# Kernel optimization log

Measured on AMD Instinct MI355X. Metric: run time of the kernel, lower is better.

The kernel has to match this reference:

```python
import jax, jax.numpy as jnp
import numpy as np

DIM = 512
HEADS = 8
LANDMARKS = 64


def setup_inputs() -> dict:
    key = jax.random.key(0)
    ks = jax.random.split(key, 9)
    B, N, C = 2, 16384, DIM
    s = 0.02
    return {
        "x": jax.random.normal(ks[0], (B, N, C), dtype=jnp.float32),
        "wq": jax.random.normal(ks[1], (C, C), dtype=jnp.float32) * s,
        "bq": jnp.zeros((C,), dtype=jnp.float32),
        "wk": jax.random.normal(ks[2], (C, C), dtype=jnp.float32) * s,
        "bk": jnp.zeros((C,), dtype=jnp.float32),
        "wv": jax.random.normal(ks[3], (C, C), dtype=jnp.float32) * s,
        "bv": jnp.zeros((C,), dtype=jnp.float32),
        "wo": jax.random.normal(ks[4], (C, C), dtype=jnp.float32) * s,
        "bo": jnp.zeros((C,), dtype=jnp.float32),
    }


def _to_heads(x, H):
    B, N, C = x.shape
    return x.reshape(B, N, H, C // H).transpose(0, 2, 1, 3)  # (B,H,N,hd)


def reference(x, wq, bq, wk, bk, wv, bv, wo, bo):
    B, N, C = x.shape
    H = HEADS
    hd = C // H
    scale = hd ** (-0.5)
    m = min(LANDMARKS, N)

    q = _to_heads(x @ wq.T + bq, H) * scale  # (B,H,N,hd)
    k = _to_heads(x @ wk.T + bk, H)
    v = _to_heads(x @ wv.T + bv, H)

    if N <= m * 2:
        attn = jax.nn.softmax(jnp.einsum("bhnd,bhkd->bhnk", q, k), axis=-1)
        out = jnp.einsum("bhnk,bhkd->bhnd", attn, v)
    else:
        seg = (N + m - 1) // m
        pad = seg * m - N
        if pad > 0:
            q_p = jnp.pad(q, ((0, 0), (0, 0), (0, pad), (0, 0)))
            k_p = jnp.pad(k, ((0, 0), (0, 0), (0, pad), (0, 0)))
        else:
            q_p, k_p = q, k
        # landmarks: mean over consecutive segments of length seg (zero-pad included, as in torch)
        q_land = q_p.reshape(B, H, m, seg, hd).mean(3)  # (B,H,m,hd)
        k_land = k_p.reshape(B, H, m, seg, hd).mean(3)

        ker1 = jax.nn.softmax(jnp.einsum("bhnd,bhmd->bhnm", q, k_land), axis=-1)  # (B,H,N,m)
        ker2 = jax.nn.softmax(jnp.einsum("bhld,bhmd->bhlm", q_land, k_land), axis=-1)  # (B,H,m,m)
        ker3 = jax.nn.softmax(jnp.einsum("bhmd,bhnd->bhmn", q_land, k), axis=-1)  # (B,H,m,N)
        ker2_inv = jnp.linalg.pinv(ker2)  # (B,H,m,m)

        kv = jnp.einsum("bhmn,bhnd->bhmd", ker3, v)  # (B,H,m,hd)
        out = jnp.einsum("bhnm,bhmd->bhnd", ker1, ker2_inv @ kv)

    out = out.transpose(0, 2, 1, 3).reshape(B, N, C)
    return out @ wo.T + bo
```

## Files before the change

kernel.cpp:

```cpp
#include <hip/hip_runtime.h>
#include <stdint.h>


constexpr int B_   = 2;
constexpr int N_   = 16384;
constexpr int C_   = 512;
constexpr int H_   = 8;
constexpr int HD_  = 64;
constexpr int LM_  = 64;
constexpr int SEG_ = 256;
constexpr int BH_  = 16;
constexpr int NCH_ = 16;
constexpr int NPART_ = 64;
constexpr int SW1_ = 3;
constexpr int SW2_ = 2;

#define RCOND_ (640.0 * 1.1920928955078125e-07)

typedef unsigned short ushort4_t __attribute__((ext_vector_type(4)));
typedef unsigned short ushort8_t __attribute__((ext_vector_type(8)));
typedef __bf16 bf16x8 __attribute__((ext_vector_type(8)));
typedef float f32x4 __attribute__((ext_vector_type(4)));

__device__ inline float bf2f(unsigned short u) {
  union { unsigned int i; float f; } x; x.i = ((unsigned int)u) << 16; return x.f;
}
__device__ inline unsigned short f2bf(float f) {
  union { float f; unsigned int i; } x; x.f = f;
  unsigned int lsb = (x.i >> 16) & 1;
  return (unsigned short)((x.i + 0x7fffu + lsb) >> 16);
}
__device__ inline bf16x8 ld_bf8(const unsigned short* p) { return *(const bf16x8*)p; }

__device__ __forceinline__ void gload_lds16(const unsigned short* gsrc, unsigned short* ldst) {
  __builtin_amdgcn_global_load_lds((const __attribute__((address_space(1))) void*)gsrc,
                                   (__attribute__((address_space(3))) void*)ldst, 16, 0, 0);
}

__global__ __launch_bounds__(256) void cvt_w4_kernel(const float* __restrict__ wq,
                                                     const float* __restrict__ wk,
                                                     const float* __restrict__ wv,
                                                     const float* __restrict__ wo,
                                                     unsigned short* __restrict__ dq,
                                                     unsigned short* __restrict__ dk,
                                                     unsigned short* __restrict__ dv,
                                                     unsigned short* __restrict__ dwo) {
  int which = blockIdx.y;
  const float* src = which == 0 ? wq : which == 1 ? wk : which == 2 ? wv : wo;
  unsigned short* dst = which == 0 ? dq : which == 1 ? dk : which == 2 ? dv : dwo;
  int i = blockIdx.x * 256 + threadIdx.x;
  const float* s = src + (size_t)i * 8;
  float4 x0 = *(const float4*)(s);
  float4 x1 = *(const float4*)(s + 4);
  ushort8_t u;
  u[0] = f2bf(x0.x); u[1] = f2bf(x0.y); u[2] = f2bf(x0.z); u[3] = f2bf(x0.w);
  u[4] = f2bf(x1.x); u[5] = f2bf(x1.y); u[6] = f2bf(x1.z); u[7] = f2bf(x1.w);
  *(ushort8_t*)(dst + (size_t)i * 8) = u;
}

__global__ __launch_bounds__(512) void seg_mean_kernel(const float* __restrict__ x,
                                                       float* __restrict__ xbar,
                                                       unsigned short* __restrict__ xb) {
  int bl = blockIdx.x;
  int b = bl / LM_, l = bl % LM_;
  int t = threadIdx.x;
  int c4 = t & 127;
  int rq = t >> 7;
  const size_t rowbase = (size_t)b * N_ + (size_t)l * SEG_;
  const float* xp = x + rowbase * C_;
  float4 s = make_float4(0.f, 0.f, 0.f, 0.f);
  for (int r = rq * 64; r < rq * 64 + 64; ++r) {
    float4 v = *(const float4*)(xp + (size_t)r * C_ + c4 * 4);
    s.x += v.x; s.y += v.y; s.z += v.z; s.w += v.w;
    ushort4_t u;
    u[0] = f2bf(v.x); u[1] = f2bf(v.y); u[2] = f2bf(v.z); u[3] = f2bf(v.w);
    *(ushort4_t*)(xb + (rowbase + r) * C_ + c4 * 4) = u;
  }
  __shared__ float red[4][512];
  *(float4*)&red[rq][c4 * 4] = s;
  __syncthreads();
  if (rq == 0) {
    float4 a0 = *(float4*)&red[0][c4 * 4];
    float4 a1 = *(float4*)&red[1][c4 * 4];
    float4 a2 = *(float4*)&red[2][c4 * 4];
    float4 a3 = *(float4*)&red[3][c4 * 4];
    const float invs = 1.0f / SEG_;
    float4 o;
    o.x = ((a0.x + a1.x) + (a2.x + a3.x)) * invs;
    o.y = ((a0.y + a1.y) + (a2.y + a3.y)) * invs;
    o.z = ((a0.z + a1.z) + (a2.z + a3.z)) * invs;
    o.w = ((a0.w + a1.w) + (a2.w + a3.w)) * invs;
    *(float4*)(xbar + (size_t)bl * C_ + c4 * 4) = o;
  }
}

__global__ __launch_bounds__(256) void land_gemm_kernel(const float* __restrict__ xbar,
                                                        const float* __restrict__ wq,
                                                        const float* __restrict__ bq,
                                                        const float* __restrict__ wk,
                                                        const float* __restrict__ bk,
                                                        float* __restrict__ qland,
                                                        float* __restrict__ kland,
                                                        unsigned short* __restrict__ qlbh,
                                                        unsigned short* __restrict__ qlbl,
                                                        unsigned short* __restrict__ klb) {
  __shared__ float As[32][68];
  __shared__ float Ws[32][68];
  int which = blockIdx.x >> 1;
  int row0 = (blockIdx.x & 1) * 64;
  int col0 = blockIdx.y * 64;
  const float* A = xbar;
  const float* W = which ? wk : wq;
  const float* bias = which ? bk : bq;
  float scale = which ? 1.0f : 0.125f;
  float* out = which ? kland : qland;
  int tid = threadIdx.x;
  int tm = tid >> 4, tn = tid & 15;
  float acc[4][4] = {};
  for (int k0 = 0; k0 < C_; k0 += 32) {
#pragma unroll
    for (int i = 0; i < 2; ++i) {
      int s = tid + i * 256;
      int r = s >> 3;
      int kg = (s & 7) << 2;
      float4 av = *(const float4*)(A + (size_t)(row0 + r) * C_ + k0 + kg);
      As[kg + 0][r] = av.x; As[kg + 1][r] = av.y;
      As[kg + 2][r] = av.z; As[kg + 3][r] = av.w;
      float4 wv = *(const float4*)(W + (size_t)(col0 + r) * C_ + k0 + kg);
      Ws[kg + 0][r] = wv.x; Ws[kg + 1][r] = wv.y;
      Ws[kg + 2][r] = wv.z; Ws[kg + 3][r] = wv.w;
    }
    __syncthreads();
#pragma unroll
    for (int kk = 0; kk < 32; ++kk) {
      float4 a = *(const float4*)&As[kk][tm * 4];
      float4 b = *(const float4*)&Ws[kk][tn * 4];
      float av[4] = {a.x, a.y, a.z, a.w};
      float bv[4] = {b.x, b.y, b.z, b.w};
#pragma unroll
      for (int i = 0; i < 4; ++i)
#pragma unroll
        for (int j = 0; j < 4; ++j) acc[i][j] += av[i] * bv[j];
    }
    __syncthreads();
  }
#pragma unroll
  for (int i = 0; i < 4; ++i) {
    int row = row0 + tm * 4 + i;
    int d0 = tn * 4;
    float o4[4];
#pragma unroll
    for (int j = 0; j < 4; ++j) o4[j] = (acc[i][j] + bias[col0 + d0 + j]) * scale;
    int b = row / LM_, n = row % LM_;
    int h = col0 >> 6;
    size_t idx = (((size_t)(b * H_ + h) * LM_) + n) * HD_ + d0;
    float4 o; o.x = o4[0]; o.y = o4[1]; o.z = o4[2]; o.w = o4[3];
    *(float4*)(out + idx) = o;
    if (which == 0) {
      ushort4_t uh, ul;
#pragma unroll
      for (int j = 0; j < 4; ++j) {
        unsigned short hbits = f2bf(o4[j]);
        uh[j] = hbits;
        ul[j] = f2bf(o4[j] - bf2f(hbits));
      }
      *(ushort4_t*)(qlbh + idx) = uh;
      *(ushort4_t*)(qlbl + idx) = ul;
    } else {
      ushort4_t uk;
#pragma unroll
      for (int j = 0; j < 4; ++j) uk[j] = f2bf(o4[j]);
      *(ushort4_t*)(klb + idx) = uk;
    }
  }
}

__device__ __forceinline__ void dma_gemm_body(const unsigned short* __restrict__ A,
                                              const unsigned short* __restrict__ W,
                                              const float* __restrict__ bias,
                                              void* __restrict__ out,
                                              float scale, int omode,
                                              int row0, int col0,
                                              unsigned short* Xs, unsigned short* Wl,
                                              int tid) {
  int w = tid >> 6, lane = tid & 63;
  int wr = w >> 1, wc = w & 1;
  f32x4 acc[4][4] = {};

  for (int k0 = 0; k0 < C_; k0 += 64) {
    __syncthreads();
#pragma unroll
    for (int i = 0; i < 4; ++i) {
      int r = i * 32 + w * 8 + (lane >> 3);
      int c8 = (lane & 7) * 8;
      gload_lds16(A + (size_t)(row0 + r) * C_ + k0 + c8, &Xs[(i * 32 + w * 8) * 64]);
      gload_lds16(W + (size_t)(col0 + r) * C_ + k0 + c8, &Wl[(i * 32 + w * 8) * 64]);
    }
    __syncthreads();
    bf16x8 af[4][2], bfr[4][2];
#pragma unroll
    for (int m = 0; m < 4; ++m) {
      af[m][0] = *(bf16x8*)&Xs[(wr * 64 + m * 16 + (lane & 15)) * 64 + (lane >> 4) * 8];
      af[m][1] = *(bf16x8*)&Xs[(wr * 64 + m * 16 + (lane & 15)) * 64 + 32 + (lane >> 4) * 8];
    }
#pragma unroll
    for (int n = 0; n < 4; ++n) {
      bfr[n][0] = *(bf16x8*)&Wl[(wc * 64 + n * 16 + (lane & 15)) * 64 + (lane >> 4) * 8];
      bfr[n][1] = *(bf16x8*)&Wl[(wc * 64 + n * 16 + (lane & 15)) * 64 + 32 + (lane >> 4) * 8];
    }
#pragma unroll
    for (int ks = 0; ks < 2; ++ks)
#pragma unroll
      for (int m = 0; m < 4; ++m)
#pragma unroll
        for (int n = 0; n < 4; ++n)
          acc[m][n] = __builtin_amdgcn_mfma_f32_16x16x32_bf16(af[m][ks], bfr[n][ks], acc[m][n], 0, 0, 0);
  }

#pragma unroll
  for (int m = 0; m < 4; ++m) {
    int rbase = row0 + wr * 64 + m * 16 + (lane >> 4) * 4;
#pragma unroll
    for (int n = 0; n < 4; ++n) {
      int c = col0 + wc * 64 + n * 16 + (lane & 15);
      float bc = bias[c];
      if (omode == 0) {
#pragma unroll
        for (int rg = 0; rg < 4; ++rg)
          ((float*)out)[(size_t)(rbase + rg) * C_ + c] = acc[m][n][rg] + bc;
      } else if (omode == 2) {
        int b = rbase >> 14, nn = rbase & 16383;
        int h = c >> 6, d = c & 63;
        ushort4_t u;
#pragma unroll
        for (int rg = 0; rg < 4; ++rg) u[rg] = f2bf((acc[m][n][rg] + bc) * scale);
        *(ushort4_t*)((unsigned short*)out + ((size_t)(b * H_ + h) * HD_ + d) * N_ + nn) = u;
      } else {
#pragma unroll
        for (int rg = 0; rg < 4; ++rg) {
          float val = (acc[m][n][rg] + bc) * scale;
          int r = rbase + rg;
          int b = r >> 14, nn = r & 16383, h = c >> 6, d = c & 63;
          ((unsigned short*)out)[(((size_t)(b * H_ + h) * N_) + nn) * HD_ + d] = f2bf(val);
        }
      }
    }
  }
}

template <int NW>
__device__ __forceinline__ void svd_sweeps(float* a, float* v, char* smemraw,
                                           int w, int lane, int nsweeps) {
  constexpr int RP = 64 / NW;
  float (*Ac)[68] = (float(*)[68])(smemraw);
  float (*Vc)[68] = (float(*)[68])(smemraw + 17408);
  float (*pg)[NW][64] = (float(*)[NW][64])(smemraw + 34816);
  float (*pa)[64] = (float(*)[64])(smemraw + 34816 + 2 * NW * 64 * 4);
  const int r0 = w * RP;
#pragma unroll
  for (int c = 0; c < RP; c += 4) {
    *(float4*)&Ac[lane][r0 + c] = make_float4(a[c], a[c + 1], a[c + 2], a[c + 3]);
    *(float4*)&Vc[lane][r0 + c] = make_float4(v[c], v[c + 1], v[c + 2], v[c + 3]);
  }

  for (int sweep = 0; sweep < nsweeps; ++sweep) {
    float p0 = 0.f, p1 = 0.f;
#pragma unroll
    for (int k = 0; k < RP; k += 2) { p0 = fmaf(a[k], a[k], p0); p1 = fmaf(a[k + 1], a[k + 1], p1); }
    pa[w][lane] = p0 + p1;
    __syncthreads();
    float alpha;
    if constexpr (NW == 4)
      alpha = (pa[0][lane] + pa[1][lane]) + (pa[2][lane] + pa[3][lane]);
    else
      alpha = ((pa[0][lane] + pa[1][lane]) + (pa[2][lane] + pa[3][lane])) +
              ((pa[4][lane] + pa[5][lane]) + (pa[6][lane] + pa[7][lane]));
    for (int mask = 1; mask < 64; ++mask) {
      int buf = mask & 1;
      int partner = lane ^ mask;
      bool lower = lane < partner;
      float beta = __shfl_xor(alpha, mask);
      float o[RP];
#pragma unroll
      for (int c = 0; c < RP; c += 4) {
        float4 t4 = *(float4*)&Ac[partner][r0 + c];
        o[c] = t4.x; o[c + 1] = t4.y; o[c + 2] = t4.z; o[c + 3] = t4.w;
      }
      float g0 = 0.f, g1 = 0.f;
#pragma unroll
      for (int k = 0; k < RP; k += 2) { g0 = fmaf(a[k], o[k], g0); g1 = fmaf(a[k + 1], o[k + 1], g1); }
      pg[buf][w][lane] = g0 + g1;
      __syncthreads();
      float gamma;
      if constexpr (NW == 4)
        gamma = (pg[buf][0][lane] + pg[buf][1][lane]) + (pg[buf][2][lane] + pg[buf][3][lane]);
      else
        gamma = ((pg[buf][0][lane] + pg[buf][1][lane]) + (pg[buf][2][lane] + pg[buf][3][lane])) +
                ((pg[buf][4][lane] + pg[buf][5][lane]) + (pg[buf][6][lane] + pg[buf][7][lane]));
      bool need = (gamma * gamma > 1e-12f * alpha * beta);
      if (__any(need)) {
        float ov[RP];
#pragma unroll
        for (int c = 0; c < RP; c += 4) {
          float4 t4 = *(float4*)&Vc[partner][r0 + c];
          ov[c] = t4.x; ov[c + 1] = t4.y; ov[c + 2] = t4.z; ov[c + 3] = t4.w;
        }
        float ap = lower ? alpha : beta;
        float aq = lower ? beta : alpha;
        float c = 1.f, s = 0.f;
        if (need) {
          float tau = (aq - ap) / (2.f * gamma);
          float t = copysignf(1.f, tau) / (fabsf(tau) + sqrtf(fmaf(tau, tau, 1.f)));
          c = rsqrtf(fmaf(t, t, 1.f));
          s = t * c;
        }
        float sm = lower ? -s : s;
#pragma unroll
        for (int k = 0; k < RP; ++k) a[k] = fmaf(sm, o[k], c * a[k]);
#pragma unroll
        for (int k = 0; k < RP; ++k) v[k] = fmaf(sm, ov[k], c * v[k]);
        float twocsg = 2.f * c * s * gamma;
        alpha = fmaf(c * c, alpha, fmaf(s * s, beta, lower ? -twocsg : twocsg));
#pragma unroll
        for (int cc = 0; cc < RP; cc += 4) {
          *(float4*)&Ac[lane][r0 + cc] = make_float4(a[cc], a[cc + 1], a[cc + 2], a[cc + 3]);
          *(float4*)&Vc[lane][r0 + cc] = make_float4(v[cc], v[cc + 1], v[cc + 2], v[cc + 3]);
        }
      }
    }
  }
}

__device__ void svd_phase1(const float* __restrict__ qland, const float* __restrict__ kland,
                           float* __restrict__ asave, float* __restrict__ vsave,
                           int bh, char* smemraw, int tid) {
  __builtin_amdgcn_s_setprio(3);
  float (*qlS)[65] = (float(*)[65])(smemraw);
  float (*klS)[65] = (float(*)[65])(smemraw + 16640);
  for (int i = 0; i < 2; ++i) {
    int s = tid + i * 512;
    int r = s >> 4, d4 = (s & 15) << 2;
    *(float4*)&qlS[r][d4] = *(const float4*)(qland + ((size_t)bh * 64 + r) * 64 + d4);
    *(float4*)&klS[r][d4] = *(const float4*)(kland + ((size_t)bh * 64 + r) * 64 + d4);
  }
  __syncthreads();
  int w = tid >> 6, lane = tid & 63;
  float a[8], v[8];
#pragma unroll
  for (int k = 0; k < 8; ++k) {
    int row = w * 8 + k;
    float acc = 0.f;
#pragma unroll
    for (int d4 = 0; d4 < 64; d4 += 4) {
      float4 qv = *(float4*)&qlS[row][d4];
      float4 kv = *(float4*)&klS[lane][d4];
      acc += qv.x * kv.x + qv.y * kv.y + qv.z * kv.z + qv.w * kv.w;
    }
    float e = expf(acc);
    float rs = e;
#pragma unroll
    for (int m = 1; m < 64; m <<= 1) rs += __shfl_xor(rs, m);
    a[k] = e * (1.f / rs);
  }
#pragma unroll
  for (int k = 0; k < 8; ++k) v[k] = (w * 8 + k == lane) ? 1.f : 0.f;
  __syncthreads();
  svd_sweeps<8>(a, v, smemraw, w, lane, SW1_);
#pragma unroll
  for (int k = 0; k < 8; ++k) {
    asave[((size_t)bh * 64 + w * 8 + k) * 64 + lane] = a[k];
    vsave[((size_t)bh * 64 + w * 8 + k) * 64 + lane] = v[k];
  }
  __builtin_amdgcn_s_setprio(0);
}

__device__ void svd_phase2(const float* __restrict__ asave, const float* __restrict__ vsave,
                           float* __restrict__ pinv, int bh, char* smemraw, int tid) {
  __builtin_amdgcn_s_setprio(3);
  double (*ps2)[64]  = (double(*)[64])(smemraw + 40960);
  float (*vsL)[65]   = (float(*)[65])(smemraw);
  float (*wasL)[65]  = (float(*)[65])(smemraw + 16640);
  int w = tid >> 6, lane = tid & 63;
  float a[8], v[8];
#pragma unroll
  for (int k = 0; k < 8; ++k) {
    a[k] = asave[((size_t)bh * 64 + w * 8 + k) * 64 + lane];
    v[k] = vsave[((size_t)bh * 64 + w * 8 + k) * 64 + lane];
  }
  svd_sweeps<8>(a, v, smemraw, w, lane, SW2_);

  double psig = 0.0;
#pragma unroll
  for (int k = 0; k < 8; ++k) psig += (double)a[k] * (double)a[k];
  ps2[w][lane] = psig;
  __syncthreads();
  double sig2 = ((ps2[0][lane] + ps2[1][lane]) + (ps2[2][lane] + ps2[3][lane])) +
                ((ps2[4][lane] + ps2[5][lane]) + (ps2[6][lane] + ps2[7][lane]));
  double smax = sig2;
#pragma unroll
  for (int m = 1; m < 64; m <<= 1) smax = fmax(smax, __shfl_xor(smax, m));
  double cutoff2 = smax * (RCOND_ * RCOND_);
  float wgt = (sig2 > cutoff2) ? (float)(1.0 / sig2) : 0.f;

#pragma unroll
  for (int k = 0; k < 8; ++k) {
    vsL[lane][w * 8 + k] = v[k];
    wasL[lane][w * 8 + k] = wgt * a[k];
  }
  __syncthreads();
  int i = tid >> 3;
  int j0 = (tid & 7) * 8;
  float acc[8] = {};
  for (int r = 0; r < 64; ++r) {
    float vv = vsL[r][i];
#pragma unroll
    for (int jj = 0; jj < 8; ++jj) acc[jj] = fmaf(vv, wasL[r][j0 + jj], acc[jj]);
  }
#pragma unroll
  for (int jj = 0; jj < 8; jj += 4) {
    float4 ovv = make_float4(acc[jj], acc[jj + 1], acc[jj + 2], acc[jj + 3]);
    *(float4*)(pinv + ((size_t)bh * 64 + i) * 64 + j0 + jj) = ovv;
  }
  __builtin_amdgcn_s_setprio(0);
}

__global__ __launch_bounds__(512) void fused1_kernel(
    const unsigned short* __restrict__ xb,
    const unsigned short* __restrict__ wqb, const float* __restrict__ bq,
    const unsigned short* __restrict__ wkb, const float* __restrict__ bk,
    const unsigned short* __restrict__ wvb, const float* __restrict__ bv,
    unsigned short* __restrict__ q4, unsigned short* __restrict__ k4,
    unsigned short* __restrict__ vt,
    const float* __restrict__ qland, const float* __restrict__ kland,
    float* __restrict__ asave, float* __restrict__ vsave) {
  __shared__ __align__(16) char smem[65536];
  int tid = threadIdx.x;
  int blk = blockIdx.x;
  if (blk < 16) { svd_phase1(qland, kland, asave, vsave, blk, smem, tid); return; }
  int g = blk - 16;
  int which = g >> 9;
  int subpair = g & 511;
  int half = tid >> 8;
  int ltid = tid & 255;
  int sub = subpair * 2 + half;
  int row0 = (sub >> 2) * 128;
  int col0 = (sub & 3) * 128;
  unsigned short* Xs = (unsigned short*)(smem + half * 32768);
  unsigned short* Wl = Xs + 128 * 64;
  if (which == 0)
    dma_gemm_body(xb, wqb, bq, q4, 0.125f, 1, row0, col0, Xs, Wl, ltid);
  else if (which == 1)
    dma_gemm_body(xb, wkb, bk, k4, 1.0f, 1, row0, col0, Xs, Wl, ltid);
  else
    dma_gemm_body(xb, wvb, bv, vt, 1.0f, 2, row0, col0, Xs, Wl, ltid);
}

__device__ void ker3kv_body(const unsigned short* __restrict__ qlh,
                            const unsigned short* __restrict__ qll,
                            const unsigned short* __restrict__ k4,
                            const unsigned short* __restrict__ vt,
                            float* __restrict__ pacc,
                            float* __restrict__ pacc0,
                            float* __restrict__ ps,
                            int bh, int ch, char* smemraw, int tid) {
  int w = tid >> 6, lane = tid & 63;
  int part = ch * 4 + w;
  int lrow = lane & 15, lgrp = lane >> 4;
  unsigned short* myP = (unsigned short*)smemraw + w * 64 * 72;

  bf16x8 qah[4][2], qal[4][2];
#pragma unroll
  for (int mf = 0; mf < 4; ++mf)
#pragma unroll
    for (int ks = 0; ks < 2; ++ks) {
      size_t off = ((size_t)bh * 64 + mf * 16 + lrow) * 64 + ks * 32 + lgrp * 8;
      qah[mf][ks] = ld_bf8(qlh + off);
      qal[mf][ks] = ld_bf8(qll + off);
    }
  bf16x8 onesf;
#pragma unroll
  for (int j = 0; j < 8; ++j) onesf[j] = (__bf16)1.0f;

  f32x4 kvacc[4][4] = {};
  f32x4 oneacc[4] = {};
  f32x4 ssum[4] = {};

  for (int sub = 0; sub < 4; ++sub) {
    int n0 = ch * 1024 + w * 256 + sub * 64;
    f32x4 sacc[4][4] = {};
#pragma unroll
    for (int ks = 0; ks < 2; ++ks) {
#pragma unroll
      for (int nf = 0; nf < 4; ++nf) {
        bf16x8 kb = ld_bf8(k4 + ((size_t)bh * N_ + n0 + nf * 16 + lrow) * 64 + ks * 32 + lgrp * 8);
#pragma unroll
        for (int mf = 0; mf < 4; ++mf) {
          sacc[mf][nf] = __builtin_amdgcn_mfma_f32_16x16x32_bf16(qah[mf][ks], kb, sacc[mf][nf], 0, 0, 0);
          sacc[mf][nf] = __builtin_amdgcn_mfma_f32_16x16x32_bf16(qal[mf][ks], kb, sacc[mf][nf], 0, 0, 0);
        }
      }
    }
#pragma unroll
    for (int mf = 0; mf < 4; ++mf) {
#pragma unroll
      for (int nf = 0; nf < 4; ++nf) {
#pragma unroll
        for (int r = 0; r < 4; ++r) {
          float pd = expf(sacc[mf][nf][r]) - 1.0f;
          ssum[mf][r] += pd;
          myP[(mf * 16 + lgrp * 4 + r) * 72 + nf * 16 + lrow] = f2bf(pd);
        }
      }
    }
#pragma unroll
    for (int ks = 0; ks < 2; ++ks) {
      bf16x8 pa[4];
#pragma unroll
      for (int mf = 0; mf < 4; ++mf)
        pa[mf] = ld_bf8(myP + (mf * 16 + lrow) * 72 + ks * 32 + lgrp * 8);
#pragma unroll
      for (int nf = 0; nf < 4; ++nf) {
        bf16x8 vb = ld_bf8(vt + ((size_t)bh * 64 + nf * 16 + lrow) * N_ + n0 + ks * 32 + lgrp * 8);
#pragma unroll
        for (int mf = 0; mf < 4; ++mf)
          kvacc[mf][nf] = __builtin_amdgcn_mfma_f32_16x16x32_bf16(pa[mf], vb, kvacc[mf][nf], 0, 0, 0);
        oneacc[nf] = __builtin_amdgcn_mfma_f32_16x16x32_bf16(onesf, vb, oneacc[nf], 0, 0, 0);
      }
    }
  }
#pragma unroll
  for (int mf = 0; mf < 4; ++mf)
#pragma unroll
    for (int m = 1; m < 16; m <<= 1)
#pragma unroll
      for (int r = 0; r < 4; ++r) ssum[mf][r] += __shfl_xor(ssum[mf][r], m);

  size_t pb = (((size_t)bh * NPART_ + part) * 64) * 64;
#pragma unroll
  for (int mf = 0; mf < 4; ++mf)
#pragma unroll
    for (int nf = 0; nf < 4; ++nf)
#pragma unroll
      for (int r = 0; r < 4; ++r)
        pacc[pb + (size_t)(mf * 16 + lgrp * 4 + r) * 64 + nf * 16 + lrow] = kvacc[mf][nf][r];
  if (lrow == 0) {
#pragma unroll
    for (int mf = 0; mf < 4; ++mf)
#pragma unroll
      for (int r = 0; r < 4; ++r)
        ps[((size_t)bh * NPART_ + part) * 64 + mf * 16 + lgrp * 4 + r] = ssum[mf][r];
  }
  if (lgrp == 0) {
#pragma unroll
    for (int nf = 0; nf < 4; ++nf)
      pacc0[((size_t)bh * NPART_ + part) * 64 + nf * 16 + lrow] = oneacc[nf][0];
  }
}

__global__ __launch_bounds__(512, 1) void fused2_kernel(
    const unsigned short* __restrict__ qlh,
    const unsigned short* __restrict__ qll,
    const unsigned short* __restrict__ k4,
    const unsigned short* __restrict__ vt,
    float* __restrict__ pacc, float* __restrict__ pacc0, float* __restrict__ ps,
    const float* __restrict__ asave, const float* __restrict__ vsave,
    float* __restrict__ pinv) {
  __shared__ __align__(16) char smem[73728];
  int tid = threadIdx.x;
  int blk = blockIdx.x;
  if (blk < 16) { svd_phase2(asave, vsave, pinv, blk, smem, tid); return; }
  int g = blk - 16;
  int bh = g >> 3, cpair = g & 7;
  int half = tid >> 8;
  int ltid = tid & 255;
  int ch = cpair * 2 + half;
  ker3kv_body(qlh, qll, k4, vt, pacc, pacc0, ps, bh, ch, smem + half * 36864, ltid);
}

__global__ __launch_bounds__(256) void cm_kernel(const float* __restrict__ pacc,
                                                 const float* __restrict__ pacc0,
                                                 const float* __restrict__ ps,
                                                 const float* __restrict__ pinv,
                                                 unsigned short* __restrict__ mtbh,
                                                 unsigned short* __restrict__ mtbl,
                                                 float* __restrict__ msum) {
  int bh = blockIdx.x;
  int tid = threadIdx.x;
  __shared__ float kvs[64][68];
  __shared__ double pcsd[64];
  for (int g = 0; g < 4; ++g) {
    int lm = g * 16 + (tid >> 4);
    int d4 = (tid & 15) * 4;
    float s = 16384.f;
    for (int part = 0; part < NPART_; ++part) s += ps[((size_t)bh * NPART_ + part) * 64 + lm];
    float4 a = make_float4(0.f, 0.f, 0.f, 0.f);
    for (int part = 0; part < NPART_; ++part) {
      float4 c0 = *(const float4*)&pacc0[((size_t)bh * NPART_ + part) * 64 + d4];
      float4 v = *(const float4*)&pacc[(((size_t)bh * NPART_ + part) * 64 + lm) * 64 + d4];
      a.x += c0.x + v.x; a.y += c0.y + v.y; a.z += c0.z + v.z; a.w += c0.w + v.w;
    }
    float inv = 1.f / s;
    kvs[lm][d4 + 0] = a.x * inv; kvs[lm][d4 + 1] = a.y * inv;
    kvs[lm][d4 + 2] = a.z * inv; kvs[lm][d4 + 3] = a.w * inv;
  }
  if (tid < 64) {
    double s = 0.0;
    for (int l = 0; l < 64; ++l) s += (double)pinv[((size_t)bh * 64 + l) * 64 + tid];
    pcsd[tid] = s;
  }
  __syncthreads();
  int l = tid >> 2, t = tid & 3;
  double o[16] = {};
  for (int j = 0; j < 64; ++j) {
    double pv = (double)pinv[((size_t)bh * 64 + l) * 64 + j];
#pragma unroll
    for (int i = 0; i < 16; ++i) o[i] += pv * (double)kvs[j][t * 16 + i];
  }
#pragma unroll
  for (int i = 0; i < 16; ++i) {
    float f = (float)o[i];
    unsigned short hi = f2bf(f);
    float lo = f - bf2f(hi);
    int d = t * 16 + i;
    mtbh[((size_t)bh * 64 + d) * 64 + l] = hi;
    mtbl[((size_t)bh * 64 + d) * 64 + l] = f2bf(lo);
  }
  if (tid < 64) {
    double m = 0.0;
    for (int j = 0; j < 64; ++j) m += pcsd[j] * (double)kvs[j][tid];
    msum[(size_t)bh * 64 + tid] = (float)(m * (1.0 / 64.0));
  }
}

__global__ __launch_bounds__(256, 1) void ker1out_mfma_kernel(
    const unsigned short* __restrict__ q4,
    const unsigned short* __restrict__ klb,
    const unsigned short* __restrict__ mtbh,
    const unsigned short* __restrict__ mtbl,
    const float* __restrict__ msum,
    unsigned short* __restrict__ outh) {
  int bh = blockIdx.y, tile = blockIdx.x;
  int b = bh >> 3, h = bh & 7;
  int tid = threadIdx.x, w = tid >> 6, lane = tid & 63;
  int lrow = lane & 15, lgrp = lane >> 4;
  int tok0 = tile * 256 + w * 64;
  __shared__ __align__(16) unsigned short Pl[4][64 * 72];
  unsigned short* myP = &Pl[w][0];

  f32x4 sacc[4][4] = {};
#pragma unroll
  for (int ks = 0; ks < 2; ++ks) {
    bf16x8 kb[4];
#pragma unroll
    for (int nf = 0; nf < 4; ++nf)
      kb[nf] = ld_bf8(klb + ((size_t)bh * 64 + nf * 16 + lrow) * 64 + ks * 32 + lgrp * 8);
#pragma unroll
    for (int mf = 0; mf < 4; ++mf) {
      bf16x8 qa = ld_bf8(q4 + ((size_t)bh * N_ + tok0 + mf * 16 + lrow) * 64 + ks * 32 + lgrp * 8);
#pragma unroll
      for (int nf = 0; nf < 4; ++nf)
        sacc[mf][nf] = __builtin_amdgcn_mfma_f32_16x16x32_bf16(qa, kb[nf], sacc[mf][nf], 0, 0, 0);
    }
  }
  f32x4 ssum[4] = {};
#pragma unroll
  for (int mf = 0; mf < 4; ++mf)
#pragma unroll
    for (int nf = 0; nf < 4; ++nf)
#pragma unroll
      for (int r = 0; r < 4; ++r) {
        sacc[mf][nf][r] = expf(sacc[mf][nf][r]);
        ssum[mf][r] += sacc[mf][nf][r];
      }
#pragma unroll
  for (int mf = 0; mf < 4; ++mf)
#pragma unroll
    for (int m = 1; m < 16; m <<= 1)
#pragma unroll
      for (int r = 0; r < 4; ++r) ssum[mf][r] += __shfl_xor(ssum[mf][r], m);
#pragma unroll
  for (int mf = 0; mf < 4; ++mf) {
    f32x4 inv;
#pragma unroll
    for (int r = 0; r < 4; ++r) inv[r] = 1.f / ssum[mf][r];
#pragma unroll
    for (int nf = 0; nf < 4; ++nf)
#pragma unroll
      for (int r = 0; r < 4; ++r) {
        float pdev = fmaf(sacc[mf][nf][r], inv[r], -0.015625f);
        myP[(mf * 16 + lgrp * 4 + r) * 72 + nf * 16 + lrow] = f2bf(pdev);
      }
  }

  f32x4 oacc[4][4] = {};
#pragma unroll
  for (int ks = 0; ks < 2; ++ks) {
    bf16x8 pa[4];
#pragma unroll
    for (int mf = 0; mf < 4; ++mf)
      pa[mf] = ld_bf8(myP + (mf * 16 + lrow) * 72 + ks * 32 + lgrp * 8);
#pragma unroll
    for (int nf = 0; nf < 4; ++nf) {
      bf16x8 mh = ld_bf8(mtbh + ((size_t)bh * 64 + nf * 16 + lrow) * 64 + ks * 32 + lgrp * 8);
      bf16x8 ml = ld_bf8(mtbl + ((size_t)bh * 64 + nf * 16 + lrow) * 64 + ks * 32 + lgrp * 8);
#pragma unroll
      for (int mf = 0; mf < 4; ++mf) {
        oacc[mf][nf] = __builtin_amdgcn_mfma_f32_16x16x32_bf16(pa[mf], mh, oacc[mf][nf], 0, 0, 0);
        oacc[mf][nf] = __builtin_amdgcn_mfma_f32_16x16x32_bf16(pa[mf], ml, oacc[mf][nf], 0, 0, 0);
      }
    }
  }
#pragma unroll
  for (int nf = 0; nf < 4; ++nf) {
    float ms = msum[(size_t)bh * 64 + nf * 16 + lrow];
#pragma unroll
    for (int mf = 0; mf < 4; ++mf)
#pragma unroll
      for (int r = 0; r < 4; ++r) {
        int tok = tok0 + mf * 16 + lgrp * 4 + r;
        int d = nf * 16 + lrow;
        outh[((size_t)b * N_ + tok) * C_ + h * HD_ + d] = f2bf(oacc[mf][nf][r] + ms);
      }
  }
}

__global__ __launch_bounds__(256) void oproj_kernel(const unsigned short* __restrict__ outh,
                                                    const unsigned short* __restrict__ wob,
                                                    const float* __restrict__ bo,
                                                    float* __restrict__ out) {
  __shared__ __align__(16) unsigned short Xs[128 * 64];
  __shared__ __align__(16) unsigned short Wl[128 * 64];
  dma_gemm_body(outh, wob, bo, out, 1.0f, 0, blockIdx.x * 128, blockIdx.y * 128,
                Xs, Wl, threadIdx.x);
}

extern "C" void kernel_launch(void* const* d_in, const int* in_sizes, int n_in,
                              void* d_out, int out_size, void* d_ws, size_t ws_size,
                              hipStream_t stream) {
  const float* x  = (const float*)d_in[0];
  const float* wq = (const float*)d_in[1];
  const float* bq = (const float*)d_in[2];
  const float* wk = (const float*)d_in[3];
  const float* bk = (const float*)d_in[4];
  const float* wv = (const float*)d_in[5];
  const float* bv = (const float*)d_in[6];
  const float* wo = (const float*)d_in[7];
  const float* bo = (const float*)d_in[8];
  float* out = (float*)d_out;

  char* base = (char*)d_ws;
  const size_t QKV = (size_t)BH_ * N_ * HD_;
  unsigned short* q4 = (unsigned short*)base;
  unsigned short* k4 = (unsigned short*)(base + QKV * 2);
  unsigned short* vt = (unsigned short*)(base + QKV * 4);
  unsigned short* outh = (unsigned short*)(base + QKV * 2);
  char* sp = base + QKV * 6;
  float* pacc  = (float*)sp; sp += (size_t)BH_ * NPART_ * 64 * 64 * 4;
  float* pacc0 = (float*)sp; sp += (size_t)BH_ * NPART_ * 64 * 4;
  float* ps    = (float*)sp; sp += (size_t)BH_ * NPART_ * 64 * 4;
  float* xbar  = (float*)sp; sp += (size_t)B_ * LM_ * C_ * 4;
  float* qland = (float*)sp; sp += (size_t)BH_ * LM_ * HD_ * 4;
  float* kland = (float*)sp; sp += (size_t)BH_ * LM_ * HD_ * 4;
  unsigned short* qlbh = (unsigned short*)sp; sp += (size_t)BH_ * LM_ * HD_ * 2;
  unsigned short* qlbl = (unsigned short*)sp; sp += (size_t)BH_ * LM_ * HD_ * 2;
  unsigned short* klb  = (unsigned short*)sp; sp += (size_t)BH_ * LM_ * HD_ * 2;
  float* pinv  = (float*)sp; sp += (size_t)BH_ * LM_ * LM_ * 4;
  unsigned short* mtbh = (unsigned short*)sp; sp += (size_t)BH_ * LM_ * HD_ * 2;
  unsigned short* mtbl = (unsigned short*)sp; sp += (size_t)BH_ * LM_ * HD_ * 2;
  float* msum  = (float*)sp; sp += (size_t)BH_ * HD_ * 4;
  float* asave = (float*)sp; sp += (size_t)BH_ * LM_ * LM_ * 4;
  float* vsave = (float*)sp; sp += (size_t)BH_ * LM_ * LM_ * 4;
  unsigned short* wob = (unsigned short*)sp; sp += (size_t)C_ * C_ * 2;
  unsigned short* wqb = (unsigned short*)sp; sp += (size_t)C_ * C_ * 2;
  unsigned short* wkb = (unsigned short*)sp; sp += (size_t)C_ * C_ * 2;
  unsigned short* wvb = (unsigned short*)sp; sp += (size_t)C_ * C_ * 2;

  unsigned short* xb = (unsigned short*)d_out;

  const int W8 = (C_ * C_) / 8;

  dim3 gc(W8 / 256, 4);
  cvt_w4_kernel<<<gc, 256, 0, stream>>>(wq, wk, wv, wo, wqb, wkb, wvb, wob);

  seg_mean_kernel<<<B_ * LM_, 512, 0, stream>>>(x, xbar, xb);
  dim3 gl(4, 8);
  land_gemm_kernel<<<gl, 256, 0, stream>>>(xbar, wq, bq, wk, bk,
                                           qland, kland, qlbh, qlbl, klb);

  fused1_kernel<<<16 + 3 * 512, 512, 0, stream>>>(
      xb, wqb, bq, wkb, bk, wvb, bv, q4, k4, vt, qland, kland, asave, vsave);

  fused2_kernel<<<16 + BH_ * 8, 512, 0, stream>>>(
      qlbh, qlbl, k4, vt, pacc, pacc0, ps, asave, vsave, pinv);

  cm_kernel<<<BH_, 256, 0, stream>>>(pacc, pacc0, ps, pinv, mtbh, mtbl, msum);

  dim3 g9(N_ / 256, BH_);
  ker1out_mfma_kernel<<<g9, 256, 0, stream>>>(q4, klb, mtbh, mtbl, msum, outh);

  dim3 g10(B_ * N_ / 128, C_ / 128);
  oproj_kernel<<<g10, 256, 0, stream>>>(outh, wob, bo, out);
}
```

Measured before the change: 385.6 us.

## Split seg-mean across columns, swizzle GEMM LDS, shuffle-based Jacobi SVD

Three separate changes. The segment-mean kernel now launches four times as many 128-thread blocks, each covering a quarter of the columns, to get more parallelism across CUs. The DMA GEMM applies an XOR swizzle to the column position in the LDS tiles so fragment reads avoid bank conflicts. The Jacobi SVD sweeps now exchange partner columns with wavefront shuffles instead of round-tripping through shared-memory arrays, which removes the LDS stores and loads inside each rotation but adds more shuffle instructions.

```diff
diff --git a/kernel.cpp b/kernel.cpp
--- a/kernel.cpp
+++ b/kernel.cpp
@@ -58,25 +58,27 @@
   *(ushort8_t*)(dst + (size_t)i * 8) = u;
 }
 
-__global__ __launch_bounds__(512) void seg_mean_kernel(const float* __restrict__ x,
+__global__ __launch_bounds__(128) void seg_mean_kernel(const float* __restrict__ x,
                                                        float* __restrict__ xbar,
                                                        unsigned short* __restrict__ xb) {
-  int bl = blockIdx.x;
+  int blk = blockIdx.x;
+  int bl = blk >> 2, cs = blk & 3;
   int b = bl / LM_, l = bl % LM_;
   int t = threadIdx.x;
-  int c4 = t & 127;
-  int rq = t >> 7;
+  int c4 = t & 31;
+  int rq = t >> 5;
+  int col = cs * 128 + c4 * 4;
   const size_t rowbase = (size_t)b * N_ + (size_t)l * SEG_;
   const float* xp = x + rowbase * C_;
   float4 s = make_float4(0.f, 0.f, 0.f, 0.f);
   for (int r = rq * 64; r < rq * 64 + 64; ++r) {
-    float4 v = *(const float4*)(xp + (size_t)r * C_ + c4 * 4);
-    s.x += v.x; s.y += v.y; s.z += v.z; s.w += v.w;
+    float4 vv = *(const float4*)(xp + (size_t)r * C_ + col);
+    s.x += vv.x; s.y += vv.y; s.z += vv.z; s.w += vv.w;
     ushort4_t u;
-    u[0] = f2bf(v.x); u[1] = f2bf(v.y); u[2] = f2bf(v.z); u[3] = f2bf(v.w);
-    *(ushort4_t*)(xb + (rowbase + r) * C_ + c4 * 4) = u;
-  }
-  __shared__ float red[4][512];
+    u[0] = f2bf(vv.x); u[1] = f2bf(vv.y); u[2] = f2bf(vv.z); u[3] = f2bf(vv.w);
+    *(ushort4_t*)(xb + (rowbase + r) * C_ + col) = u;
+  }
+  __shared__ float red[4][128];
   *(float4*)&red[rq][c4 * 4] = s;
   __syncthreads();
   if (rq == 0) {
@@ -90,7 +92,7 @@
     o.y = ((a0.y + a1.y) + (a2.y + a3.y)) * invs;
     o.z = ((a0.z + a1.z) + (a2.z + a3.z)) * invs;
     o.w = ((a0.w + a1.w) + (a2.w + a3.w)) * invs;
-    *(float4*)(xbar + (size_t)bl * C_ + c4 * 4) = o;
+    *(float4*)(xbar + (size_t)bl * C_ + col) = o;
   }
 }
 
@@ -192,21 +194,25 @@
 #pragma unroll
     for (int i = 0; i < 4; ++i) {
       int r = i * 32 + w * 8 + (lane >> 3);
-      int c8 = (lane & 7) * 8;
+      int c8 = ((lane & 7) ^ (lane >> 3)) * 8;
       gload_lds16(A + (size_t)(row0 + r) * C_ + k0 + c8, &Xs[(i * 32 + w * 8) * 64]);
       gload_lds16(W + (size_t)(col0 + r) * C_ + k0 + c8, &Wl[(i * 32 + w * 8) * 64]);
     }
     __syncthreads();
+    int cs0 = (((lane >> 4) + 0) ^ (lane & 7)) * 8;
+    int cs1 = (((lane >> 4) + 4) ^ (lane & 7)) * 8;
     bf16x8 af[4][2], bfr[4][2];
 #pragma unroll
     for (int m = 0; m < 4; ++m) {
-      af[m][0] = *(bf16x8*)&Xs[(wr * 64 + m * 16 + (lane & 15)) * 64 + (lane >> 4) * 8];
-      af[m][1] = *(bf16x8*)&Xs[(wr * 64 + m * 16 + (lane & 15)) * 64 + 32 + (lane >> 4) * 8];
+      int rb = (wr * 64 + m * 16 + (lane & 15)) * 64;
+      af[m][0] = *(bf16x8*)&Xs[rb + cs0];
+      af[m][1] = *(bf16x8*)&Xs[rb + cs1];
     }
 #pragma unroll
     for (int n = 0; n < 4; ++n) {
-      bfr[n][0] = *(bf16x8*)&Wl[(wc * 64 + n * 16 + (lane & 15)) * 64 + (lane >> 4) * 8];
-      bfr[n][1] = *(bf16x8*)&Wl[(wc * 64 + n * 16 + (lane & 15)) * 64 + 32 + (lane >> 4) * 8];
+      int rb = (wc * 64 + n * 16 + (lane & 15)) * 64;
+      bfr[n][0] = *(bf16x8*)&Wl[rb + cs0];
+      bfr[n][1] = *(bf16x8*)&Wl[rb + cs1];
     }
 #pragma unroll
     for (int ks = 0; ks < 2; ++ks)
@@ -252,16 +258,8 @@
 __device__ __forceinline__ void svd_sweeps(float* a, float* v, char* smemraw,
                                            int w, int lane, int nsweeps) {
   constexpr int RP = 64 / NW;
-  float (*Ac)[68] = (float(*)[68])(smemraw);
-  float (*Vc)[68] = (float(*)[68])(smemraw + 17408);
-  float (*pg)[NW][64] = (float(*)[NW][64])(smemraw + 34816);
-  float (*pa)[64] = (float(*)[64])(smemraw + 34816 + 2 * NW * 64 * 4);
-  const int r0 = w * RP;
-#pragma unroll
-  for (int c = 0; c < RP; c += 4) {
-    *(float4*)&Ac[lane][r0 + c] = make_float4(a[c], a[c + 1], a[c + 2], a[c + 3]);
-    *(float4*)&Vc[lane][r0 + c] = make_float4(v[c], v[c + 1], v[c + 2], v[c + 3]);
-  }
+  float (*pg)[NW][64] = (float(*)[NW][64])(smemraw);
+  float (*pa)[64] = (float(*)[64])(smemraw + 2 * NW * 64 * 4);
 
   for (int sweep = 0; sweep < nsweeps; ++sweep) {
     float p0 = 0.f, p1 = 0.f;
@@ -282,10 +280,7 @@
       float beta = __shfl_xor(alpha, mask);
       float o[RP];
 #pragma unroll
-      for (int c = 0; c < RP; c += 4) {
-        float4 t4 = *(float4*)&Ac[partner][r0 + c];
-        o[c] = t4.x; o[c + 1] = t4.y; o[c + 2] = t4.z; o[c + 3] = t4.w;
-      }
+      for (int k = 0; k < RP; ++k) o[k] = __shfl_xor(a[k], mask);
       float g0 = 0.f, g1 = 0.f;
 #pragma unroll
       for (int k = 0; k < RP; k += 2) { g0 = fmaf(a[k], o[k], g0); g1 = fmaf(a[k + 1], o[k + 1], g1); }
@@ -301,10 +296,7 @@
       if (__any(need)) {
         float ov[RP];
 #pragma unroll
-        for (int c = 0; c < RP; c += 4) {
-          float4 t4 = *(float4*)&Vc[partner][r0 + c];
-          ov[c] = t4.x; ov[c + 1] = t4.y; ov[c + 2] = t4.z; ov[c + 3] = t4.w;
-        }
+        for (int k = 0; k < RP; ++k) ov[k] = __shfl_xor(v[k], mask);
         float ap = lower ? alpha : beta;
         float aq = lower ? beta : alpha;
         float c = 1.f, s = 0.f;
@@ -321,11 +313,6 @@
         for (int k = 0; k < RP; ++k) v[k] = fmaf(sm, ov[k], c * v[k]);
         float twocsg = 2.f * c * s * gamma;
         alpha = fmaf(c * c, alpha, fmaf(s * s, beta, lower ? -twocsg : twocsg));
-#pragma unroll
-        for (int cc = 0; cc < RP; cc += 4) {
-          *(float4*)&Ac[lane][r0 + cc] = make_float4(a[cc], a[cc + 1], a[cc + 2], a[cc + 3]);
-          *(float4*)&Vc[lane][r0 + cc] = make_float4(v[cc], v[cc + 1], v[cc + 2], v[cc + 3]);
-        }
       }
     }
   }
@@ -782,7 +769,7 @@
   dim3 gc(W8 / 256, 4);
   cvt_w4_kernel<<<gc, 256, 0, stream>>>(wq, wk, wv, wo, wqb, wkb, wvb, wob);
 
-  seg_mean_kernel<<<B_ * LM_, 512, 0, stream>>>(x, xbar, xb);
+  seg_mean_kernel<<<B_ * LM_ * 4, 128, 0, stream>>>(x, xbar, xb);
   dim3 gl(4, 8);
   land_gemm_kernel<<<gl, 256, 0, stream>>>(xbar, wq, bq, wk, bk,
                                            qland, kland, qlbh, qlbl, klb);
```

Measured after the change: 398.3 us. +3.3%, slower.
